# Kernel optimization log

Hardware: AMD Instinct MI355X
Metric: run time of the kernel (lower is better)

Reference implementation:

```python
import jax, jax.numpy as jnp
import numpy as np
from jax import lax

EPS = 1e-3  # Keras BatchNormalization default epsilon


def _hard_sigmoid(x):
    # Keras recurrent_activation default for ConvLSTM2D
    return jnp.clip(0.2 * x + 0.5, 0.0, 1.0)


def _conv(x, w, padding):
    # x: [B, Cin, H, W], w: [Cout, Cin, kh, kw]
    return lax.conv_general_dilated(
        x, w, window_strides=(1, 1), padding=padding,
        dimension_numbers=("NCHW", "OIHW", "NCHW"))


def _sympad(x):
    # tf.pad(..., [[0,0],[0,0],[0,0],[1,1],[1,1]], 'SYMMETRIC') on [B,T,C,H,W]
    return jnp.pad(x, ((0, 0), (0, 0), (0, 0), (1, 1), (1, 1)), mode="symmetric")


def _convlstm(xpad, h0, c0, W, U, b):
    # xpad: [B, T, Cin, H+2, W+2]; input conv 'VALID' -> HxW; recurrent conv 'SAME'.
    # Keras gate order along the 4F channel axis: i, f, c(g), o.
    # activation='sigmoid' (candidate/output), recurrent_activation=hard_sigmoid.
    def step(carry, x_t):
        h, c = carry
        z = _conv(x_t, W, "VALID") + _conv(h, U, "SAME") + b[None, :, None, None]
        i, f, g, o = jnp.split(z, 4, axis=1)
        c_new = _hard_sigmoid(f) * c + _hard_sigmoid(i) * jax.nn.sigmoid(g)
        h_new = _hard_sigmoid(o) * jax.nn.sigmoid(c_new)
        return (h_new, c_new), h_new

    (hT, cT), hs = lax.scan(step, (h0, c0), jnp.moveaxis(xpad, 1, 0))
    return jnp.moveaxis(hs, 0, 1), hT, cT  # [B,T,F,H,W], [B,F,H,W] x2


def setup_inputs() -> dict:
    key = jax.random.key(0)
    ks = jax.random.split(key, 5)
    B, T, C, H, Wd, F = 4, 12, 4, 60, 80, 64
    z = lambda: jnp.zeros((B, F, H, Wd), jnp.float32)
    return {
        "inputs": jax.random.normal(ks[0], (B, T, C, H, Wd), jnp.float32),
        "h1_0": z(), "c1_0": z(), "h2_0": z(), "c2_0": z(),
        "W1": jax.random.normal(ks[1], (4 * F, C, 3, 3), jnp.float32) * 0.05,
        "U1": jax.random.normal(ks[2], (4 * F, F, 3, 3), jnp.float32) * 0.05,
        "b1": jnp.zeros((4 * F,), jnp.float32),
        "W2": jax.random.normal(ks[3], (4 * F, F, 3, 3), jnp.float32) * 0.05,
        "U2": jax.random.normal(ks[4], (4 * F, F, 3, 3), jnp.float32) * 0.05,
        "b2": jnp.zeros((4 * F,), jnp.float32),
        "gamma": jnp.ones((Wd,), jnp.float32),
        "beta": jnp.zeros((Wd,), jnp.float32),
    }


def reference(inputs, h1_0, c1_0, h2_0, c2_0, W1, U1, b1, W2, U2, b2, gamma, beta):
    x, h1, c1 = _convlstm(_sympad(inputs), h1_0, c1_0, W1, U1, b1)
    # BatchNorm, Keras default axis=-1 (the W axis here), training-mode batch stats.
    mean = jnp.mean(x, axis=(0, 1, 2, 3), keepdims=True)
    var = jnp.var(x, axis=(0, 1, 2, 3), keepdims=True)
    x = (x - mean) * lax.rsqrt(var + EPS) * gamma + beta
    x, h2, c2 = _convlstm(_sympad(x), h2_0, c2_0, W2, U2, b2)
    # dropout treated as identity (deterministic reference)
    return (x, h1, c1, h2, c2)
```

## Files before the change

kernel.cpp:

```cpp
#include <hip/hip_runtime.h>
#include <hip/hip_bf16.h>

typedef __hip_bfloat16 bf16;
typedef __attribute__((ext_vector_type(8))) short sh8;
typedef __attribute__((ext_vector_type(4))) short sh4;
typedef __attribute__((ext_vector_type(4))) float f32x4;

#define HWp 4800
#define Wd 80
#define Hd 60
#define Fh 64
#define Bn 4
#define Tn 12
#define KYS 5248
#define sHT ((long)Fh*HWp)
#define ZT  ((long)Fh*HWp*4)

__device__ __forceinline__ float b2f(bf16 v){ return __bfloat162float(v); }
__device__ __forceinline__ bf16 f2b(float v){ return __float2bfloat16(v); }
__device__ __forceinline__ float bits2f(short s){
    return __uint_as_float(((unsigned)(unsigned short)s) << 16);
}
__device__ __forceinline__ short f2bits(float f){
    bf16 t = f2b(f); short s; __builtin_memcpy(&s, &t, 2); return s;
}

__global__ void perm_w_kernel(const float* __restrict__ src, float* __restrict__ dst, int cin){
    int idx = blockIdx.x*256 + threadIdx.x;
    int n = 256*cin*9;
    if (idx >= n) return;
    int co = idx/(cin*9); int r = idx - co*(cin*9);
    int g = co >> 6, fo = co & 63;
    dst[(fo*4+g)*cin*9 + r] = src[idx];
}
__global__ void perm_bias_kernel(const float* __restrict__ src, float* __restrict__ dst){
    int idx = threadIdx.x;
    int g = idx >> 6, fo = idx & 63;
    dst[fo*4+g] = src[idx];
}
__global__ void pack_w_kernel(const float* __restrict__ U, short* __restrict__ Apk){
    int d = blockIdx.x*256 + threadIdx.x;
    if (d >= 147456) return;
    int j = d & 7, l = (d>>3) & 63, ct = (d>>9) & 15, oc = d >> 13;
    int o = oc >> 1, cc = oc & 1;
    int co = ct*16 + (l & 15);
    int ci = cc*32 + (l>>4)*8 + j;
    Apk[d] = f2bits(U[(co*Fh + ci)*9 + o]);
}

__global__ void copy_f32_kernel(const float* __restrict__ src, float* __restrict__ dst, int n){
    int idx = blockIdx.x*256+threadIdx.x;
    if (idx < n) dst[idx] = src[idx];
}
__global__ void copy_h_f32_kernel(const float* __restrict__ src, long bstride, float* __restrict__ dst){
    long idx = (long)blockIdx.x*256+threadIdx.x;
    long n = (long)Bn*Fh*HWp;
    if (idx >= n) return;
    long b = idx/(Fh*HWp); long r = idx - b*(Fh*HWp);
    dst[idx] = src[b*bstride + r];
}
__global__ void h0cl_kernel(const float* __restrict__ src, bf16* __restrict__ dst){
    long idx = (long)blockIdx.x*256 + threadIdx.x;
    if (idx >= (long)Bn*Fh*HWp) return;
    int fo = (int)(idx & 63);
    long rest = idx >> 6;
    int p = (int)(rest % HWp);
    int b = (int)(rest / HWp);
    dst[idx] = f2b(src[((long)b*Fh + fo)*HWp + p]);
}

__global__ void zx1_kernel(const float* __restrict__ xin,
                           const float* __restrict__ Wf,
                           const float* __restrict__ bias,
                           short* __restrict__ zx)
{
    int p = blockIdx.x*blockDim.x + threadIdx.x;
    if (p >= HWp) return;
    int fo = blockIdx.y, bt = blockIdx.z;
    int y = p / Wd, x = p - y*Wd;
    const float* wf = Wf + fo*4*4*9;
    float acc[4] = {bias[fo*4+0], bias[fo*4+1], bias[fo*4+2], bias[fo*4+3]};
    int ym = (y > 0 ? y-1 : 0)*Wd, y0 = y*Wd, yp = (y < Hd-1 ? y+1 : Hd-1)*Wd;
    int xm = (x > 0 ? x-1 : 0),    xp = (x < Wd-1 ? x+1 : Wd-1);
    for (int ci = 0; ci < 4; ++ci){
        const float* ic = xin + ((long)bt*4 + ci)*HWp;
        float v[9];
        v[0]=ic[ym+xm]; v[1]=ic[ym+x]; v[2]=ic[ym+xp];
        v[3]=ic[y0+xm]; v[4]=ic[y0+x]; v[5]=ic[y0+xp];
        v[6]=ic[yp+xm]; v[7]=ic[yp+x]; v[8]=ic[yp+xp];
        #pragma unroll
        for (int g = 0; g < 4; ++g){
            const float* w = wf + (g*4+ci)*9;
            acc[g] += v[0]*w[0]+v[1]*w[1]+v[2]*w[2]
                    + v[3]*w[3]+v[4]*w[4]+v[5]*w[5]
                    + v[6]*w[6]+v[7]*w[7]+v[8]*w[8];
        }
    }
    sh4 o4 = { f2bits(acc[0]), f2bits(acc[1]), f2bits(acc[2]), f2bits(acc[3]) };
    *(sh4*)(zx + (((long)bt*Fh + fo)*HWp + p)*4) = o4;
}

template<bool CLAMP, int NT>
__device__ __forceinline__ void stage_cl(const short* __restrict__ src, int y, short* lt){
    const int tid = threadIdx.x;
    for (int n = tid; n < 1968; n += NT){
        int row = n/656, rem = n - row*656;
        int rg = y + row - 1;
        bool rvalid = CLAMP ? true : (rg >= 0 && rg < Hd);
        rg = min(max(rg,0), Hd-1);
        int xg, cc, xl; bool cvalid = true;
        if (rem < 640){ xg = rem>>3; cc = rem&7; xl = xg+1; }
        else if (rem < 648){ xg = 0; cc = rem-640; xl = 0; cvalid = CLAMP; }
        else { xg = Wd-1; cc = rem-648; xl = 81; cvalid = CLAMP; }
        sh8 v = {0,0,0,0,0,0,0,0};
        if (rvalid && cvalid) v = *(const sh8*)(src + ((long)(rg*Wd + xg)*64 + cc*8));
        *(sh8*)(lt + row*KYS + xl*64 + ((cc ^ (xl&7))<<3)) = v;
    }
}

__device__ __forceinline__ void gemm_core(const short* __restrict__ Apk, const short* lt,
                                          int wv, int lane, f32x4 acc[4][5]){
    const int lane15 = lane & 15, grp = lane >> 4;
    #pragma unroll
    for (int o = 0; o < 9; ++o){
        int ky = o/3, kx = o - 3*(o/3);
        const short* lk = lt + ky*KYS;
        #pragma unroll
        for (int c = 0; c < 2; ++c){
            sh8 bfr[5];
            #pragma unroll
            for (int pt = 0; pt < 5; ++pt){
                int xl = pt*16 + lane15 + kx;
                int cc = (c*4 + grp) ^ (xl & 7);
                bfr[pt] = *(const sh8*)(lk + xl*64 + cc*8);
            }
            const short* ab = Apk + ((long)((o*2 + c)*16 + wv))*512 + lane*8;
            #pragma unroll
            for (int g = 0; g < 4; ++g){
                sh8 af = *(const sh8*)(ab + (long)g*4*512);
                #pragma unroll
                for (int pt = 0; pt < 5; ++pt)
                    acc[g][pt] = __builtin_amdgcn_mfma_f32_16x16x32_bf16(af, bfr[pt], acc[g][pt], 0, 0, 0);
            }
        }
    }
}

template<bool WRITE_FX>
__global__ __launch_bounds__(128) void rec_step(
    const bf16* __restrict__ hprev, long h_bstride,
    const short* __restrict__ Upk,
    const short* __restrict__ zx_t, long z_bstride,
    float* __restrict__ c,
    bf16* __restrict__ hout,
    float* __restrict__ fx, long f_bstride)
{
    __shared__ short lt[3*KYS];
    __shared__ short lo[80*36];
    int y = blockIdx.x, b = blockIdx.y, fh = blockIdx.z;
    int tid = threadIdx.x, lane = tid & 63, wv = tid >> 6;
    int lane15 = lane & 15, grp = lane >> 4;
    int ft = fh*2 + wv;

    stage_cl<false,128>((const short*)hprev + (long)b*h_bstride, y, lt);

    sh4 zq[5][4]; float cold[5][4];
    const short* zb = zx_t + (long)b*z_bstride;
    #pragma unroll
    for (int pt = 0; pt < 5; ++pt){
        int p = y*Wd + pt*16 + lane15;
        #pragma unroll
        for (int r = 0; r < 4; ++r){
            int fo = ft*16 + grp*4 + r;
            zq[pt][r] = *(const sh4*)(zb + ((long)fo*HWp + p)*4);
            cold[pt][r] = c[((long)b*Fh + fo)*HWp + p];
        }
    }
    __syncthreads();

    f32x4 acc[4][5];
    #pragma unroll
    for (int g = 0; g < 4; ++g)
        #pragma unroll
        for (int pt = 0; pt < 5; ++pt) acc[g][pt] = (f32x4){0.f,0.f,0.f,0.f};

    #pragma unroll
    for (int o = 0; o < 9; ++o){
        int ky = o/3, kx = o - 3*(o/3);
        const short* lk = lt + ky*KYS;
        #pragma unroll
        for (int cch = 0; cch < 2; ++cch){
            sh8 bfr[5];
            #pragma unroll
            for (int pt = 0; pt < 5; ++pt){
                int xl = pt*16 + lane15 + kx;
                int cc = (cch*4 + grp) ^ (xl & 7);
                bfr[pt] = *(const sh8*)(lk + xl*64 + cc*8);
            }
            const short* ab = Upk + ((long)((o*2 + cch)*16 + ft))*512 + lane*8;
            #pragma unroll
            for (int g = 0; g < 4; ++g){
                sh8 af = *(const sh8*)(ab + (long)g*4*512);
                #pragma unroll
                for (int pt = 0; pt < 5; ++pt)
                    acc[g][pt] = __builtin_amdgcn_mfma_f32_16x16x32_bf16(af, bfr[pt], acc[g][pt], 0, 0, 0);
            }
        }
    }

    #pragma unroll
    for (int pt = 0; pt < 5; ++pt){
        int pl = pt*16 + lane15;
        int p = y*Wd + pl;
        #pragma unroll
        for (int r = 0; r < 4; ++r){
            int fo = ft*16 + grp*4 + r;
            float zi = acc[0][pt][r] + bits2f(zq[pt][r][0]);
            float zf = acc[1][pt][r] + bits2f(zq[pt][r][1]);
            float zg = acc[2][pt][r] + bits2f(zq[pt][r][2]);
            float zo = acc[3][pt][r] + bits2f(zq[pt][r][3]);
            float gi = fminf(fmaxf(0.2f*zi+0.5f, 0.f), 1.f);
            float gf = fminf(fmaxf(0.2f*zf+0.5f, 0.f), 1.f);
            float go = fminf(fmaxf(0.2f*zo+0.5f, 0.f), 1.f);
            float sg = 1.f/(1.f+__expf(-zg));
            float cn = gf*cold[pt][r] + gi*sg;
            float hn = go * (1.f/(1.f+__expf(-cn)));
            c[((long)b*Fh + fo)*HWp + p] = cn;
            lo[pl*36 + wv*16 + grp*4 + r] = f2bits(hn);
            if (WRITE_FX)
                fx[(long)b*f_bstride + (long)fo*HWp + p] = hn;
        }
    }
    __syncthreads();
    short* hb = (short*)hout + (long)b*sHT;
    #pragma unroll
    for (int k = 0; k < 5; ++k){
        int e = k*128 + tid;
        int pl = e >> 3, f4 = (e & 7)*4;
        sh4 hv = *(const sh4*)(lo + pl*36 + f4);
        *(sh4*)(hb + (long)(y*Wd + pl)*64 + fh*32 + f4) = hv;
    }
}

__global__ __launch_bounds__(256,2) void zx_mfma(
    const bf16* __restrict__ x1,
    const short* __restrict__ Wpk,
    const float* __restrict__ bias,
    short* __restrict__ zxb)
{
    __shared__ short lt[3*KYS];
    int y = blockIdx.x, img = blockIdx.y;
    int t = img / Bn, b = img - t*Bn;
    int tid = threadIdx.x, lane = tid & 63, wv = tid >> 6;
    int lane15 = lane & 15, grp = lane >> 4;
    stage_cl<true,256>((const short*)x1 + (long)img*sHT, y, lt);
    __syncthreads();
    f32x4 acc[4][5];
    #pragma unroll
    for (int g = 0; g < 4; ++g)
        #pragma unroll
        for (int pt = 0; pt < 5; ++pt) acc[g][pt] = (f32x4){0.f,0.f,0.f,0.f};
    gemm_core(Wpk, lt, wv, lane, acc);
    short* zb = zxb + ((long)(b*Tn + t))*ZT;
    #pragma unroll
    for (int pt = 0; pt < 5; ++pt){
        int p = y*Wd + pt*16 + lane15;
        #pragma unroll
        for (int r = 0; r < 4; ++r){
            int fo = wv*16 + grp*4 + r;
            sh4 o4 = { f2bits(acc[0][pt][r] + bias[fo]),
                       f2bits(acc[1][pt][r] + bias[64+fo]),
                       f2bits(acc[2][pt][r] + bias[128+fo]),
                       f2bits(acc[3][pt][r] + bias[192+fo]) };
            *(sh4*)(zb + ((long)fo*HWp + p)*4) = o4;
        }
    }
}

#define BN_GRID 480
__global__ void bn_sum_cl(const short* __restrict__ x, float* __restrict__ sums){
    __shared__ float ls[160];
    int tid = threadIdx.x;
    if (tid < 160) ls[tid] = 0.f;
    __syncthreads();
    long gid = (long)blockIdx.x*256 + tid;
    const long nchunk = (long)Bn*Tn*HWp*8;
    float s = 0.f, q = 0.f;
    for (long ch = gid; ch < nchunk; ch += (long)BN_GRID*256){
        sh8 v = *(const sh8*)(x + ch*8);
        #pragma unroll
        for (int j = 0; j < 8; ++j){ float f = bits2f(v[j]); s += f; q += f*f; }
    }
    int w = (int)((gid>>3) % Wd);
    atomicAdd(&ls[w], s); atomicAdd(&ls[80+w], q);
    __syncthreads();
    if (tid < 160) atomicAdd(&sums[tid], ls[tid]);
}
__global__ void bn_coef_kernel(const float* __restrict__ sums, const float* __restrict__ g,
                               const float* __restrict__ bt, float* __restrict__ coef){
    int w = threadIdx.x;
    const float N = (float)(Bn*Tn*Fh*Hd);
    float mean = sums[w]/N;
    float var  = sums[80+w]/N - mean*mean;
    float sc = rsqrtf(var + 1e-3f)*g[w];
    coef[w] = sc;
    coef[80+w] = bt[w] - mean*sc;
}
__global__ void bn_apply_cl(short* __restrict__ x, const float* __restrict__ coef){
    long gid = (long)blockIdx.x*256 + threadIdx.x;
    const long nchunk = (long)Bn*Tn*HWp*8;
    int w = (int)((gid>>3) % Wd);
    float sc = coef[w], sh = coef[80+w];
    for (long ch = gid; ch < nchunk; ch += (long)BN_GRID*256){
        sh8 v = *(sh8*)(x + ch*8);
        #pragma unroll
        for (int j = 0; j < 8; ++j) v[j] = f2bits(bits2f(v[j])*sc + sh);
        *(sh8*)(x + ch*8) = v;
    }
}

extern "C" void kernel_launch(void* const* d_in, const int* in_sizes, int n_in,
                              void* d_out, int out_size, void* d_ws, size_t ws_size,
                              hipStream_t stream){
    const float* xin  = (const float*)d_in[0];
    const float* h1_0 = (const float*)d_in[1];
    const float* c1_0 = (const float*)d_in[2];
    const float* h2_0 = (const float*)d_in[3];
    const float* c2_0 = (const float*)d_in[4];
    const float* W1   = (const float*)d_in[5];
    const float* U1   = (const float*)d_in[6];
    const float* b1   = (const float*)d_in[7];
    const float* W2   = (const float*)d_in[8];
    const float* U2   = (const float*)d_in[9];
    const float* b2   = (const float*)d_in[10];
    const float* gamma= (const float*)d_in[11];
    const float* beta = (const float*)d_in[12];
    float* out = (float*)d_out;

    char* ws = (char*)d_ws;
    float* W1f = (float*)ws; ws += (size_t)256*4*9*4;
    float* b1f = (float*)ws; ws += 1024;
    short* U1p = (short*)ws; ws += (size_t)147456*2;
    short* W2p = (short*)ws; ws += (size_t)147456*2;
    short* U2p = (short*)ws; ws += (size_t)147456*2;
    float* sums= (float*)ws; ws += 1024;
    float* coef= (float*)ws; ws += 1024;
    float* cbuf= (float*)ws; ws += (size_t)Bn*Fh*HWp*4;
    bf16*  h0b = (bf16*)ws; ws += (size_t)Bn*Fh*HWp*2;
    bf16*  hdb = (bf16*)ws; ws += (size_t)2*Bn*Fh*HWp*2;
    bf16*  x1  = (bf16*)ws; ws += (size_t)Bn*Tn*Fh*HWp*2;
    short* zx  = (short*)ws; ws += (size_t)Bn*Tn*256*HWp*2;

    const long nImg = (long)Bn*Fh*HWp;
    const long xOff = (long)Bn*Tn*Fh*HWp;
    int nImgB = (int)((nImg+255)/256);

    perm_w_kernel<<<(256*4*9+255)/256, 256, 0, stream>>>(W1, W1f, 4);
    perm_bias_kernel<<<1,256,0,stream>>>(b1, b1f);
    pack_w_kernel<<<576,256,0,stream>>>(U1, U1p);
    pack_w_kernel<<<576,256,0,stream>>>(W2, W2p);
    pack_w_kernel<<<576,256,0,stream>>>(U2, U2p);

    dim3 rgrid(Hd, Bn, 2);
    const long zbstr = (long)Tn*ZT;

    dim3 zgrid1((HWp+255)/256, 64, Bn*Tn);
    zx1_kernel<<<zgrid1,256,0,stream>>>(xin, W1f, b1f, zx);
    copy_f32_kernel<<<nImgB,256,0,stream>>>(c1_0, cbuf, (int)nImg);
    h0cl_kernel<<<nImgB,256,0,stream>>>(h1_0, h0b);
    for (int t = 0; t < Tn; ++t){
        const bf16* hp = (t==0) ? h0b : x1 + (long)(t-1)*Bn*sHT;
        bf16* ho = x1 + (long)t*Bn*sHT;
        if (t == Tn-1)
            rec_step<true><<<rgrid,128,0,stream>>>(hp, sHT, U1p,
                zx + (long)t*ZT, zbstr, cbuf, ho, out + xOff, sHT);
        else
            rec_step<false><<<rgrid,128,0,stream>>>(hp, sHT, U1p,
                zx + (long)t*ZT, zbstr, cbuf, ho, nullptr, 0);
    }
    copy_f32_kernel<<<nImgB,256,0,stream>>>(cbuf, out + xOff + nImg, (int)nImg);

    hipMemsetAsync(sums, 0, 640, stream);
    bn_sum_cl<<<BN_GRID,256,0,stream>>>((const short*)x1, sums);
    bn_coef_kernel<<<1,80,0,stream>>>(sums, gamma, beta, coef);
    bn_apply_cl<<<BN_GRID,256,0,stream>>>((short*)x1, coef);

    dim3 zgrid2(Hd, Bn*Tn);
    zx_mfma<<<zgrid2,256,0,stream>>>(x1, W2p, b2, zx);
    copy_f32_kernel<<<nImgB,256,0,stream>>>(c2_0, cbuf, (int)nImg);
    h0cl_kernel<<<nImgB,256,0,stream>>>(h2_0, h0b);
    for (int t = 0; t < Tn; ++t){
        const bf16* hp = (t==0) ? h0b : hdb + (long)((t-1)&1)*Bn*sHT;
        bf16* ho = hdb + (long)(t&1)*Bn*sHT;
        rec_step<true><<<rgrid,128,0,stream>>>(hp, sHT, U2p,
            zx + (long)t*ZT, zbstr, cbuf, ho, out + (long)t*sHT, (long)Tn*sHT);
    }
    copy_h_f32_kernel<<<nImgB,256,0,stream>>>(out + (long)(Tn-1)*sHT, (long)Tn*sHT, out + xOff + 2*nImg);
    copy_f32_kernel<<<nImgB,256,0,stream>>>(cbuf, out + xOff + 3*nImg, (int)nImg);
}
```

Measured before the change: 1.004 ms.

## Replace per-timestep recurrent launches with persistent kernel using grid barrier

Replaces the 12 per-timestep rec_step launches per layer with one persistent kernel of 240 blocks that loops over time, syncing through a global atomic barrier between steps. The cell state stays in registers across timesteps, which removes the cbuf round-trips and the separate copy kernels. Final h and c are written directly to the outputs. The cost is fewer, larger blocks (256 threads, one per row and batch), so less parallelism per step, plus spin-wait overhead. The barrier relies on all blocks being co-resident and has a spin timeout.

Result: slower. 1.896 ms (+88.8%).

```diff
diff --git a/kernel.cpp b/kernel.cpp
--- a/kernel.cpp
+++ b/kernel.cpp
@@ -15,6 +15,7 @@
 #define KYS 5248
 #define sHT ((long)Fh*HWp)
 #define ZT  ((long)Fh*HWp*4)
+#define NBLK (Hd*Bn)
 
 __device__ __forceinline__ float b2f(bf16 v){ return __bfloat162float(v); }
 __device__ __forceinline__ bf16 f2b(float v){ return __float2bfloat16(v); }
@@ -48,17 +49,6 @@
     Apk[d] = f2bits(U[(co*Fh + ci)*9 + o]);
 }
 
-__global__ void copy_f32_kernel(const float* __restrict__ src, float* __restrict__ dst, int n){
-    int idx = blockIdx.x*256+threadIdx.x;
-    if (idx < n) dst[idx] = src[idx];
-}
-__global__ void copy_h_f32_kernel(const float* __restrict__ src, long bstride, float* __restrict__ dst){
-    long idx = (long)blockIdx.x*256+threadIdx.x;
-    long n = (long)Bn*Fh*HWp;
-    if (idx >= n) return;
-    long b = idx/(Fh*HWp); long r = idx - b*(Fh*HWp);
-    dst[idx] = src[b*bstride + r];
-}
 __global__ void h0cl_kernel(const float* __restrict__ src, bf16* __restrict__ dst){
     long idx = (long)blockIdx.x*256 + threadIdx.x;
     if (idx >= (long)Bn*Fh*HWp) return;
@@ -146,99 +136,125 @@
     }
 }
 
-template<bool WRITE_FX>
-__global__ __launch_bounds__(128) void rec_step(
-    const bf16* __restrict__ hprev, long h_bstride,
+template<int LAYER>
+__global__ __launch_bounds__(256,1) void rec_persist(
+    const bf16* __restrict__ h0,
     const short* __restrict__ Upk,
-    const short* __restrict__ zx_t, long z_bstride,
-    float* __restrict__ c,
-    bf16* __restrict__ hout,
-    float* __restrict__ fx, long f_bstride)
+    const short* __restrict__ zxall,
+    const float* __restrict__ cin,
+    bf16* __restrict__ hbuf,
+    float* __restrict__ fX,
+    float* __restrict__ fH,
+    float* __restrict__ fC,
+    unsigned* __restrict__ bar)
 {
     __shared__ short lt[3*KYS];
-    __shared__ short lo[80*36];
-    int y = blockIdx.x, b = blockIdx.y, fh = blockIdx.z;
+    __shared__ short lo[80*68];
+    int bid = blockIdx.x;
+    int y = bid % Hd, b = bid / Hd;
     int tid = threadIdx.x, lane = tid & 63, wv = tid >> 6;
     int lane15 = lane & 15, grp = lane >> 4;
-    int ft = fh*2 + wv;
-
-    stage_cl<false,128>((const short*)hprev + (long)b*h_bstride, y, lt);
-
-    sh4 zq[5][4]; float cold[5][4];
-    const short* zb = zx_t + (long)b*z_bstride;
+
+    float creg[5][4];
     #pragma unroll
     for (int pt = 0; pt < 5; ++pt){
         int p = y*Wd + pt*16 + lane15;
         #pragma unroll
         for (int r = 0; r < 4; ++r){
-            int fo = ft*16 + grp*4 + r;
-            zq[pt][r] = *(const sh4*)(zb + ((long)fo*HWp + p)*4);
-            cold[pt][r] = c[((long)b*Fh + fo)*HWp + p];
-        }
-    }
-    __syncthreads();
-
-    f32x4 acc[4][5];
-    #pragma unroll
-    for (int g = 0; g < 4; ++g)
-        #pragma unroll
-        for (int pt = 0; pt < 5; ++pt) acc[g][pt] = (f32x4){0.f,0.f,0.f,0.f};
-
-    #pragma unroll
-    for (int o = 0; o < 9; ++o){
-        int ky = o/3, kx = o - 3*(o/3);
-        const short* lk = lt + ky*KYS;
-        #pragma unroll
-        for (int cch = 0; cch < 2; ++cch){
-            sh8 bfr[5];
-            #pragma unroll
-            for (int pt = 0; pt < 5; ++pt){
-                int xl = pt*16 + lane15 + kx;
-                int cc = (cch*4 + grp) ^ (xl & 7);
-                bfr[pt] = *(const sh8*)(lk + xl*64 + cc*8);
-            }
-            const short* ab = Upk + ((long)((o*2 + cch)*16 + ft))*512 + lane*8;
-            #pragma unroll
-            for (int g = 0; g < 4; ++g){
-                sh8 af = *(const sh8*)(ab + (long)g*4*512);
-                #pragma unroll
-                for (int pt = 0; pt < 5; ++pt)
-                    acc[g][pt] = __builtin_amdgcn_mfma_f32_16x16x32_bf16(af, bfr[pt], acc[g][pt], 0, 0, 0);
-            }
+            int fo = wv*16 + grp*4 + r;
+            creg[pt][r] = cin[((long)b*Fh + fo)*HWp + p];
+        }
+    }
+
+    for (int t = 0; t < Tn; ++t){
+        const short* hp;
+        if (t == 0) hp = (const short*)h0 + (long)b*sHT;
+        else if (LAYER == 1) hp = (const short*)hbuf + ((long)(t-1)*Bn + b)*sHT;
+        else hp = (const short*)hbuf + ((long)((t-1)&1)*Bn + b)*sHT;
+
+        sh4 zq[5][4];
+        const short* zb = zxall + ((long)b*Tn + t)*ZT;
+        #pragma unroll
+        for (int pt = 0; pt < 5; ++pt){
+            int p = y*Wd + pt*16 + lane15;
+            #pragma unroll
+            for (int r = 0; r < 4; ++r){
+                int fo = wv*16 + grp*4 + r;
+                zq[pt][r] = *(const sh4*)(zb + ((long)fo*HWp + p)*4);
+            }
+        }
+
+        stage_cl<false,256>(hp, y, lt);
+        __syncthreads();
+
+        f32x4 acc[4][5];
+        #pragma unroll
+        for (int g = 0; g < 4; ++g)
+            #pragma unroll
+            for (int pt = 0; pt < 5; ++pt) acc[g][pt] = (f32x4){0.f,0.f,0.f,0.f};
+        gemm_core(Upk, lt, wv, lane, acc);
+
+        #pragma unroll
+        for (int pt = 0; pt < 5; ++pt){
+            int pl = pt*16 + lane15;
+            int p = y*Wd + pl;
+            #pragma unroll
+            for (int r = 0; r < 4; ++r){
+                int fo = wv*16 + grp*4 + r;
+                float zi = acc[0][pt][r] + bits2f(zq[pt][r][0]);
+                float zf = acc[1][pt][r] + bits2f(zq[pt][r][1]);
+                float zg = acc[2][pt][r] + bits2f(zq[pt][r][2]);
+                float zo = acc[3][pt][r] + bits2f(zq[pt][r][3]);
+                float gi = fminf(fmaxf(0.2f*zi+0.5f, 0.f), 1.f);
+                float gf = fminf(fmaxf(0.2f*zf+0.5f, 0.f), 1.f);
+                float go = fminf(fmaxf(0.2f*zo+0.5f, 0.f), 1.f);
+                float sg = 1.f/(1.f+__expf(-zg));
+                float cn = gf*creg[pt][r] + gi*sg;
+                float hn = go * (1.f/(1.f+__expf(-cn)));
+                creg[pt][r] = cn;
+                lo[pl*68 + wv*16 + grp*4 + r] = f2bits(hn);
+                if (LAYER == 2)
+                    fX[((long)(b*Tn + t)*Fh + fo)*HWp + p] = hn;
+                if (t == Tn-1)
+                    fH[((long)b*Fh + fo)*HWp + p] = hn;
+            }
+        }
+        __syncthreads();
+        short* hb = (LAYER == 1)
+            ? (short*)hbuf + ((long)t*Bn + b)*sHT
+            : (short*)hbuf + ((long)(t&1)*Bn + b)*sHT;
+        #pragma unroll
+        for (int k = 0; k < 5; ++k){
+            int e = k*256 + tid;
+            int pl = e >> 4, f4 = (e & 15)*4;
+            *(sh4*)(hb + (long)(y*Wd + pl)*64 + f4) = *(const sh4*)(lo + pl*68 + f4);
+        }
+
+        if (t < Tn-1){
+            __threadfence();
+            __syncthreads();
+            if (tid == 0){
+                __hip_atomic_fetch_add(bar, 1u, __ATOMIC_ACQ_REL, __HIP_MEMORY_SCOPE_AGENT);
+                unsigned target = (unsigned)(NBLK*(t+1));
+                long spins = 0;
+                while (__hip_atomic_load(bar, __ATOMIC_ACQUIRE, __HIP_MEMORY_SCOPE_AGENT) < target){
+                    __builtin_amdgcn_s_sleep(2);
+                    if (++spins > 50000000L) break;
+                }
+            }
+            __syncthreads();
+            __threadfence();
         }
     }
 
     #pragma unroll
     for (int pt = 0; pt < 5; ++pt){
-        int pl = pt*16 + lane15;
-        int p = y*Wd + pl;
+        int p = y*Wd + pt*16 + lane15;
         #pragma unroll
         for (int r = 0; r < 4; ++r){
-            int fo = ft*16 + grp*4 + r;
-            float zi = acc[0][pt][r] + bits2f(zq[pt][r][0]);
-            float zf = acc[1][pt][r] + bits2f(zq[pt][r][1]);
-            float zg = acc[2][pt][r] + bits2f(zq[pt][r][2]);
-            float zo = acc[3][pt][r] + bits2f(zq[pt][r][3]);
-            float gi = fminf(fmaxf(0.2f*zi+0.5f, 0.f), 1.f);
-            float gf = fminf(fmaxf(0.2f*zf+0.5f, 0.f), 1.f);
-            float go = fminf(fmaxf(0.2f*zo+0.5f, 0.f), 1.f);
-            float sg = 1.f/(1.f+__expf(-zg));
-            float cn = gf*cold[pt][r] + gi*sg;
-            float hn = go * (1.f/(1.f+__expf(-cn)));
-            c[((long)b*Fh + fo)*HWp + p] = cn;
-            lo[pl*36 + wv*16 + grp*4 + r] = f2bits(hn);
-            if (WRITE_FX)
-                fx[(long)b*f_bstride + (long)fo*HWp + p] = hn;
-        }
-    }
-    __syncthreads();
-    short* hb = (short*)hout + (long)b*sHT;
-    #pragma unroll
-    for (int k = 0; k < 5; ++k){
-        int e = k*128 + tid;
-        int pl = e >> 3, f4 = (e & 7)*4;
-        sh4 hv = *(const sh4*)(lo + pl*36 + f4);
-        *(sh4*)(hb + (long)(y*Wd + pl)*64 + fh*32 + f4) = hv;
+            int fo = wv*16 + grp*4 + r;
+            fC[((long)b*Fh + fo)*HWp + p] = creg[pt][r];
+        }
     }
 }
 
@@ -345,7 +361,7 @@
     short* U2p = (short*)ws; ws += (size_t)147456*2;
     float* sums= (float*)ws; ws += 1024;
     float* coef= (float*)ws; ws += 1024;
-    float* cbuf= (float*)ws; ws += (size_t)Bn*Fh*HWp*4;
+    unsigned* bar = (unsigned*)ws; ws += 1024;
     bf16*  h0b = (bf16*)ws; ws += (size_t)Bn*Fh*HWp*2;
     bf16*  hdb = (bf16*)ws; ws += (size_t)2*Bn*Fh*HWp*2;
     bf16*  x1  = (bf16*)ws; ws += (size_t)Bn*Tn*Fh*HWp*2;
@@ -360,25 +376,13 @@
     pack_w_kernel<<<576,256,0,stream>>>(U1, U1p);
     pack_w_kernel<<<576,256,0,stream>>>(W2, W2p);
     pack_w_kernel<<<576,256,0,stream>>>(U2, U2p);
-
-    dim3 rgrid(Hd, Bn, 2);
-    const long zbstr = (long)Tn*ZT;
+    hipMemsetAsync(bar, 0, 8, stream);
 
     dim3 zgrid1((HWp+255)/256, 64, Bn*Tn);
     zx1_kernel<<<zgrid1,256,0,stream>>>(xin, W1f, b1f, zx);
-    copy_f32_kernel<<<nImgB,256,0,stream>>>(c1_0, cbuf, (int)nImg);
     h0cl_kernel<<<nImgB,256,0,stream>>>(h1_0, h0b);
-    for (int t = 0; t < Tn; ++t){
-        const bf16* hp = (t==0) ? h0b : x1 + (long)(t-1)*Bn*sHT;
-        bf16* ho = x1 + (long)t*Bn*sHT;
-        if (t == Tn-1)
-            rec_step<true><<<rgrid,128,0,stream>>>(hp, sHT, U1p,
-                zx + (long)t*ZT, zbstr, cbuf, ho, out + xOff, sHT);
-        else
-            rec_step<false><<<rgrid,128,0,stream>>>(hp, sHT, U1p,
-                zx + (long)t*ZT, zbstr, cbuf, ho, nullptr, 0);
-    }
-    copy_f32_kernel<<<nImgB,256,0,stream>>>(cbuf, out + xOff + nImg, (int)nImg);
+    rec_persist<1><<<NBLK,256,0,stream>>>(h0b, U1p, zx, c1_0,
+        x1, nullptr, out + xOff, out + xOff + nImg, bar + 0);
 
     hipMemsetAsync(sums, 0, 640, stream);
     bn_sum_cl<<<BN_GRID,256,0,stream>>>((const short*)x1, sums);
@@ -387,14 +391,7 @@
 
     dim3 zgrid2(Hd, Bn*Tn);
     zx_mfma<<<zgrid2,256,0,stream>>>(x1, W2p, b2, zx);
-    copy_f32_kernel<<<nImgB,256,0,stream>>>(c2_0, cbuf, (int)nImg);
     h0cl_kernel<<<nImgB,256,0,stream>>>(h2_0, h0b);
-    for (int t = 0; t < Tn; ++t){
-        const bf16* hp = (t==0) ? h0b : hdb + (long)((t-1)&1)*Bn*sHT;
-        bf16* ho = hdb + (long)(t&1)*Bn*sHT;
-        rec_step<true><<<rgrid,128,0,stream>>>(hp, sHT, U2p,
-            zx + (long)t*ZT, zbstr, cbuf, ho, out + (long)t*sHT, (long)Tn*sHT);
-    }
-    copy_h_f32_kernel<<<nImgB,256,0,stream>>>(out + (long)(Tn-1)*sHT, (long)Tn*sHT, out + xOff + 2*nImg);
-    copy_f32_kernel<<<nImgB,256,0,stream>>>(cbuf, out + xOff + 3*nImg, (int)nImg);
-}
+    rec_persist<2><<<NBLK,256,0,stream>>>(h0b, U2p, zx, c2_0,
+        hdb, out, out + xOff + 2*nImg, out + xOff + 3*nImg, bar + 1);
+}
```
